# Kernel tuning notes

Hardware: AMD Instinct MI355X
Metric: run time of the kernel (lower is better)

## Reference

```python
import jax, jax.numpy as jnp
import numpy as np

N, F_IN, H = 8192, 128, 256
AVG_DEG_P = 16.0 / N  # ~16 neighbors per node, BA-graph-like sparsity


def setup_inputs() -> dict:
    key = jax.random.key(0)
    ks = jax.random.split(key, 16)
    # symmetric 0/1 adjacency, no self-loops
    B = jax.random.bernoulli(ks[0], AVG_DEG_P, (N, N)).astype(jnp.float32)
    A = jnp.maximum(B, B.T)
    A = A * (1.0 - jnp.eye(N, dtype=jnp.float32))
    features = jax.random.normal(ks[1], (N, F_IN), dtype=jnp.float32)
    treatments = jax.random.bernoulli(ks[2], 0.1, (N, 1)).astype(jnp.float32)
    def glorot(k, shape):
        lim = float(np.sqrt(6.0 / (shape[0] + shape[1])))
        return jax.random.uniform(k, shape, jnp.float32, -lim, lim)
    return {
        "A": A,
        "features": features,
        "treatments": treatments,
        "W1": glorot(ks[3], (F_IN, H)),   # GCNConv layer 1 weight
        "b1": jnp.zeros((H,), jnp.float32),
        "W2": glorot(ks[4], (H, H)),      # GCNConv layer 2 weight
        "b2": jnp.zeros((H,), jnp.float32),
        "W_emb": glorot(ks[5], (H + 1, H)),
        "b_emb": jnp.zeros((H,), jnp.float32),
        "W_t0": glorot(ks[6], (H, 1)),
        "b_t0": jnp.zeros((1,), jnp.float32),
        "W_t1": glorot(ks[7], (H, 1)),
        "b_t1": jnp.zeros((1,), jnp.float32),
    }


def _gcn_norm(A):
    # PyG GCNConv default: D^-1/2 (A + I) D^-1/2
    A_hat = A + jnp.eye(A.shape[0], dtype=A.dtype)
    d = jnp.sum(A_hat, axis=1)
    dinv = jnp.where(d > 0, 1.0 / jnp.sqrt(d), 0.0)
    return A_hat * dinv[:, None] * dinv[None, :]


def reference(A, features, treatments, W1, b1, W2, b2, W_emb, b_emb, W_t0, b_t0, W_t1, b_t1):
    nA = _gcn_norm(A)                                  # [N, N]
    h = jax.nn.relu(nA @ (features @ W1) + b1)         # GCNConv 1, [N, H]
    h = jax.nn.relu(nA @ (h @ W2) + b2)                # GCNConv 2, [N, H]
    deg = jnp.sum(A, axis=1) + 1e-8                    # [N]
    # faithful to torch: (A * treatments).sum(dim=1) broadcasts treatments[N,1] over columns
    exposure = (jnp.sum(A * treatments, axis=1) / deg)[:, None]  # [N, 1]
    rep = jnp.concatenate([h, exposure], axis=1)       # [N, H+1]
    emb = jax.nn.relu(rep @ W_emb + b_emb)             # [N, H]
    y0_pred = (emb @ W_t0 + b_t0).reshape(-1)          # [N]
    y1_pred = (emb @ W_t1 + b_t1).reshape(-1)          # [N]
    return (y0_pred, y1_pred, emb)
```

## Files before the change

kernel.cpp:

```cpp
#include <hip/hip_runtime.h>

#define NN   8192
#define FIN  128
#define HH   256
#define CAP  128

typedef float f32x4 __attribute__((ext_vector_type(4)));

__device__ __forceinline__ const f32x4* c4(const float* p) { return (const f32x4*)p; }
__device__ __forceinline__       f32x4* p4(float* p)       { return (f32x4*)p; }

__device__ __forceinline__ void build_body(
    int row, const float* __restrict__ A, const float* __restrict__ treat,
    int* __restrict__ cols, int* __restrict__ cnt,
    float* __restrict__ dinv, float* __restrict__ expo,
    int* s_cnt, float* s_rs)
{
  const f32x4* Ar = c4(A + (size_t)row * NN);
  if (threadIdx.x == 0) *s_cnt = 0;
  __syncthreads();

  float rs = 0.f;
  int* myCols = cols + (size_t)row * CAP;
  #pragma unroll
  for (int it = 0; it < NN / 4 / 256; ++it) {
    const int idx = it * 256 + threadIdx.x;
    const f32x4 a = __builtin_nontemporal_load(Ar + idx);
    const int base = idx * 4;
    #pragma unroll
    for (int u = 0; u < 4; ++u) {
      if (a[u] != 0.0f) {
        rs += a[u];
        int p = atomicAdd(s_cnt, 1);
        if (p < CAP) myCols[p] = base + u;
      }
    }
  }
  #pragma unroll
  for (int off = 32; off > 0; off >>= 1) rs += __shfl_down(rs, off);
  const int wid = threadIdx.x >> 6;
  if ((threadIdx.x & 63) == 0) s_rs[wid] = rs;
  __syncthreads();
  if (threadIdx.x == 0) {
    const float R = s_rs[0] + s_rs[1] + s_rs[2] + s_rs[3];
    int n = *s_cnt; if (n > CAP) n = CAP;
    cnt[row]  = n;
    dinv[row] = rsqrtf(R + 1.0f);
    expo[row] = treat[row] * R / (R + 1e-8f);
  }
}

template<int K, bool EXPO, bool HEADS>
__device__ __forceinline__ void gemm_body(
    int bidx,
    const float* __restrict__ M, const float* __restrict__ W,
    const float* __restrict__ bias, const float* __restrict__ expo,
    const float* __restrict__ Wt0, const float* __restrict__ Wt1,
    float* __restrict__ out, float* __restrict__ y0, float* __restrict__ y1,
    float (*As)[64], float (*Bs)[64])
{
  const int tid = threadIdx.x;
  const int tx = tid & 15, ty = tid >> 4;
  const int bx = bidx & 127, by = bidx >> 7;
  const int r0 = bx * 64, c0 = by * 64;
  const int la_r = tid & 63;
  const int la_k = (tid >> 6) << 2;
  const int lb_k = tid >> 4;
  const int lb_c = (tid & 15) << 2;

  const float* Abase = M + (size_t)(r0 + la_r) * K + la_k;
  const float* Bbase = W + (size_t)lb_k * HH + c0 + lb_c;

  f32x4 aR = *c4(Abase);
  f32x4 bR = *c4(Bbase);
  float acc[4][4] = {};

  #pragma unroll 1
  for (int k0 = 0; k0 < K; k0 += 16) {
    As[la_k + 0][la_r] = aR[0];
    As[la_k + 1][la_r] = aR[1];
    As[la_k + 2][la_r] = aR[2];
    As[la_k + 3][la_r] = aR[3];
    *p4(&Bs[lb_k][lb_c]) = bR;
    __syncthreads();
    if (k0 + 16 < K) {
      aR = *c4(Abase + k0 + 16);
      bR = *c4(Bbase + (size_t)(k0 + 16) * HH);
    }
    #pragma unroll
    for (int kk = 0; kk < 16; ++kk) {
      const f32x4 av = *c4(&As[kk][ty * 4]);
      const f32x4 bv = *c4(&Bs[kk][tx * 4]);
      #pragma unroll
      for (int i = 0; i < 4; ++i)
        #pragma unroll
        for (int j = 0; j < 4; ++j)
          acc[i][j] += av[i] * bv[j];
    }
    __syncthreads();
  }

  f32x4 eb = {0.f, 0.f, 0.f, 0.f}, bs = {0.f, 0.f, 0.f, 0.f};
  if constexpr (EXPO) {
    eb = *c4(&W[(size_t)K * HH + c0 + tx * 4]);
    bs = *c4(&bias[c0 + tx * 4]);
  }
  f32x4 wt0 = {0.f, 0.f, 0.f, 0.f}, wt1 = {0.f, 0.f, 0.f, 0.f};
  if constexpr (HEADS) {
    wt0 = *c4(&Wt0[c0 + tx * 4]);
    wt1 = *c4(&Wt1[c0 + tx * 4]);
  }
  #pragma unroll
  for (int i = 0; i < 4; ++i) {
    const int r = r0 + ty * 4 + i;
    f32x4 o;
    if constexpr (EXPO) {
      const float e = expo[r];
      #pragma unroll
      for (int j = 0; j < 4; ++j) o[j] = fmaxf(acc[i][j] + e * eb[j] + bs[j], 0.f);
    } else {
      #pragma unroll
      for (int j = 0; j < 4; ++j) o[j] = acc[i][j];
    }
    *p4(&out[(size_t)r * HH + c0 + tx * 4]) = o;
    if constexpr (HEADS) {
      float s0 = o[0] * wt0[0] + o[1] * wt0[1] + o[2] * wt0[2] + o[3] * wt0[3];
      float s1 = o[0] * wt1[0] + o[1] * wt1[1] + o[2] * wt1[2] + o[3] * wt1[3];
      #pragma unroll
      for (int off = 8; off > 0; off >>= 1) {
        s0 += __shfl_down(s0, off);
        s1 += __shfl_down(s1, off);
      }
      if ((tid & 15) == 0) {
        atomicAdd(&y0[r], s0);
        atomicAdd(&y1[r], s1);
      }
    }
  }
}

__global__ __launch_bounds__(256) void k_build_gemm1(
    const float* __restrict__ A, const float* __restrict__ treat,
    const float* __restrict__ feats, const float* __restrict__ W1,
    int* __restrict__ cols, int* __restrict__ cnt,
    float* __restrict__ dinv, float* __restrict__ expo,
    float* __restrict__ bufA)
{
  __shared__ float As[16][64];
  __shared__ float Bs[16][64];
  __shared__ int   s_cnt;
  __shared__ float s_rs[4];
  const int b = blockIdx.x;
  if (b < 512) {
    gemm_body<FIN, false, false>(b, feats, W1, nullptr, nullptr, nullptr, nullptr,
                                 bufA, nullptr, nullptr, As, Bs);
  } else {
    build_body(b - 512, A, treat, cols, cnt, dinv, expo, &s_cnt, s_rs);
  }
}

template<int K, bool EXPO, bool HEADS>
__global__ __launch_bounds__(256) void k_gemm(
    const float* __restrict__ M, const float* __restrict__ W,
    const float* __restrict__ bias, const float* __restrict__ expo,
    const float* __restrict__ Wt0, const float* __restrict__ Wt1,
    float* __restrict__ out, float* __restrict__ y0, float* __restrict__ y1)
{
  __shared__ float As[16][64];
  __shared__ float Bs[16][64];
  gemm_body<K, EXPO, HEADS>(blockIdx.x, M, W, bias, expo, Wt0, Wt1, out, y0, y1, As, Bs);
}

template<bool INIT>
__global__ __launch_bounds__(256) void k_agg(
    const float* __restrict__ M,
    const int* __restrict__ cols, const int* __restrict__ cnt,
    const float* __restrict__ dinv, const float* __restrict__ bias,
    float* __restrict__ out,
    float* __restrict__ dout, const float* __restrict__ bt0, const float* __restrict__ bt1)
{
  const int wid  = threadIdx.x >> 6;
  const int lane = threadIdx.x & 63;
  const int i    = blockIdx.x * 4 + wid;
  __shared__ int   s_cols[4][CAP];
  __shared__ float s_w[4][CAP];

  if constexpr (INIT) {
    if (blockIdx.x < 64) {
      const int idx = blockIdx.x * 256 + threadIdx.x;
      dout[idx] = (idx < NN) ? bt0[0] : bt1[0];
    }
  }

  const int n = cnt[i];
  if (lane < n) {
    const int j = cols[(size_t)i * CAP + lane];
    s_cols[wid][lane] = j;  s_w[wid][lane] = dinv[j];
  }
  if (lane + 64 < n) {
    const int j = cols[(size_t)i * CAP + lane + 64];
    s_cols[wid][lane + 64] = j;  s_w[wid][lane + 64] = dinv[j];
  }
  __syncthreads();

  const float di = dinv[i];
  const f32x4 bias4 = *c4(&bias[lane * 4]);
  f32x4 acc = *c4(&M[(size_t)i * HH + lane * 4]);
  acc *= di;
  #pragma unroll 4
  for (int t = 0; t < n; ++t) {
    const int   j = s_cols[wid][t];
    const float w = s_w[wid][t];
    const f32x4 v = *c4(&M[(size_t)j * HH + lane * 4]);
    acc += w * v;
  }
  f32x4 o = di * acc + bias4;
  #pragma unroll
  for (int q = 0; q < 4; ++q) o[q] = fmaxf(o[q], 0.f);
  *p4(&out[(size_t)i * HH + lane * 4]) = o;
}

extern "C" void kernel_launch(void* const* d_in, const int* in_sizes, int n_in,
                              void* d_out, int out_size, void* d_ws, size_t ws_size,
                              hipStream_t stream)
{
  const float* A      = (const float*)d_in[0];
  const float* feats  = (const float*)d_in[1];
  const float* treat  = (const float*)d_in[2];
  const float* W1     = (const float*)d_in[3];
  const float* b1     = (const float*)d_in[4];
  const float* W2     = (const float*)d_in[5];
  const float* b2     = (const float*)d_in[6];
  const float* W_emb  = (const float*)d_in[7];
  const float* b_emb  = (const float*)d_in[8];
  const float* W_t0   = (const float*)d_in[9];
  const float* b_t0   = (const float*)d_in[10];
  const float* W_t1   = (const float*)d_in[11];
  const float* b_t1   = (const float*)d_in[12];
  float* dout = (float*)d_out;

  int*   cols = (int*)d_ws;
  int*   cnt  = cols + (size_t)NN * CAP;
  float* dinv = (float*)(cnt + NN);
  float* expo = dinv + NN;
  float* bufA = expo + NN;
  float* bufB = bufA + (size_t)NN * HH;

  float* y0  = dout;
  float* y1  = dout + NN;
  float* emb = dout + 2 * NN;

  k_build_gemm1<<<8704, 256, 0, stream>>>(A, treat, feats, W1, cols, cnt, dinv, expo, bufA);
  k_agg<false><<<NN / 4, 256, 0, stream>>>(bufA, cols, cnt, dinv, b1, bufB,
                                           nullptr, nullptr, nullptr);
  k_gemm<HH, false, false><<<512, 256, 0, stream>>>(bufB, W2, nullptr, nullptr,
                                                    nullptr, nullptr, bufA, nullptr, nullptr);
  k_agg<true><<<NN / 4, 256, 0, stream>>>(bufA, cols, cnt, dinv, b2, bufB,
                                          dout, b_t0, b_t1);
  k_gemm<HH, true, true><<<512, 256, 0, stream>>>(bufB, W_emb, b_emb, expo,
                                                  W_t0, W_t1, emb, y0, y1);
}
```

Before: 458.4 us.

## Reorder GCN layer 1 to aggregate 128-wide features before the W1 GEMM

Result: faster. 441.0 us (-3.8%).

```diff
diff --git a/kernel.cpp b/kernel.cpp
--- a/kernel.cpp
+++ b/kernel.cpp
@@ -6,18 +6,23 @@
 #define CAP  128
 
 typedef float f32x4 __attribute__((ext_vector_type(4)));
+typedef float f32x2 __attribute__((ext_vector_type(2)));
 
 __device__ __forceinline__ const f32x4* c4(const float* p) { return (const f32x4*)p; }
 __device__ __forceinline__       f32x4* p4(float* p)       { return (f32x4*)p; }
-
-__device__ __forceinline__ void build_body(
-    int row, const float* __restrict__ A, const float* __restrict__ treat,
+__device__ __forceinline__ const f32x2* c2(const float* p) { return (const f32x2*)p; }
+__device__ __forceinline__       f32x2* p2(float* p)       { return (f32x2*)p; }
+
+__global__ __launch_bounds__(256) void k_build(
+    const float* __restrict__ A, const float* __restrict__ treat,
     int* __restrict__ cols, int* __restrict__ cnt,
-    float* __restrict__ dinv, float* __restrict__ expo,
-    int* s_cnt, float* s_rs)
-{
+    float* __restrict__ dinv, float* __restrict__ expo)
+{
+  const int row = blockIdx.x;
   const f32x4* Ar = c4(A + (size_t)row * NN);
-  if (threadIdx.x == 0) *s_cnt = 0;
+  __shared__ int   s_cnt;
+  __shared__ float s_rs[4];
+  if (threadIdx.x == 0) s_cnt = 0;
   __syncthreads();
 
   float rs = 0.f;
@@ -31,7 +36,7 @@
     for (int u = 0; u < 4; ++u) {
       if (a[u] != 0.0f) {
         rs += a[u];
-        int p = atomicAdd(s_cnt, 1);
+        int p = atomicAdd(&s_cnt, 1);
         if (p < CAP) myCols[p] = base + u;
       }
     }
@@ -43,14 +48,48 @@
   __syncthreads();
   if (threadIdx.x == 0) {
     const float R = s_rs[0] + s_rs[1] + s_rs[2] + s_rs[3];
-    int n = *s_cnt; if (n > CAP) n = CAP;
+    int n = s_cnt; if (n > CAP) n = CAP;
     cnt[row]  = n;
     dinv[row] = rsqrtf(R + 1.0f);
     expo[row] = treat[row] * R / (R + 1e-8f);
   }
 }
 
-template<int K, bool EXPO, bool HEADS>
+__global__ __launch_bounds__(256) void k_agg0(
+    const float* __restrict__ X,
+    const int* __restrict__ cols, const int* __restrict__ cnt,
+    const float* __restrict__ dinv, float* __restrict__ out)
+{
+  const int wid  = threadIdx.x >> 6;
+  const int lane = threadIdx.x & 63;
+  const int i    = blockIdx.x * 4 + wid;
+  __shared__ int   s_cols[4][CAP];
+  __shared__ float s_w[4][CAP];
+
+  const int n = cnt[i];
+  if (lane < n) {
+    const int j = cols[(size_t)i * CAP + lane];
+    s_cols[wid][lane] = j;  s_w[wid][lane] = dinv[j];
+  }
+  if (lane + 64 < n) {
+    const int j = cols[(size_t)i * CAP + lane + 64];
+    s_cols[wid][lane + 64] = j;  s_w[wid][lane + 64] = dinv[j];
+  }
+  __syncthreads();
+
+  const float di = dinv[i];
+  f32x2 acc = *c2(&X[(size_t)i * FIN + lane * 2]);
+  acc *= di;
+  #pragma unroll 4
+  for (int t = 0; t < n; ++t) {
+    const int   j = s_cols[wid][t];
+    const float w = s_w[wid][t];
+    acc += w * (*c2(&X[(size_t)j * FIN + lane * 2]));
+  }
+  *p2(&out[(size_t)i * FIN + lane * 2]) = di * acc;
+}
+
+template<int K, bool RELU, bool EXPO, bool HEADS>
 __device__ __forceinline__ void gemm_body(
     int bidx,
     const float* __restrict__ M, const float* __restrict__ W,
@@ -101,10 +140,8 @@
   }
 
   f32x4 eb = {0.f, 0.f, 0.f, 0.f}, bs = {0.f, 0.f, 0.f, 0.f};
-  if constexpr (EXPO) {
-    eb = *c4(&W[(size_t)K * HH + c0 + tx * 4]);
-    bs = *c4(&bias[c0 + tx * 4]);
-  }
+  if constexpr (RELU) bs = *c4(&bias[c0 + tx * 4]);
+  if constexpr (EXPO) eb = *c4(&W[(size_t)K * HH + c0 + tx * 4]);
   f32x4 wt0 = {0.f, 0.f, 0.f, 0.f}, wt1 = {0.f, 0.f, 0.f, 0.f};
   if constexpr (HEADS) {
     wt0 = *c4(&Wt0[c0 + tx * 4]);
@@ -114,10 +151,15 @@
   for (int i = 0; i < 4; ++i) {
     const int r = r0 + ty * 4 + i;
     f32x4 o;
-    if constexpr (EXPO) {
-      const float e = expo[r];
-      #pragma unroll
-      for (int j = 0; j < 4; ++j) o[j] = fmaxf(acc[i][j] + e * eb[j] + bs[j], 0.f);
+    if constexpr (RELU) {
+      float e = 0.f;
+      if constexpr (EXPO) e = expo[r];
+      #pragma unroll
+      for (int j = 0; j < 4; ++j) {
+        float v = acc[i][j] + bs[j];
+        if constexpr (EXPO) v += e * eb[j];
+        o[j] = fmaxf(v, 0.f);
+      }
     } else {
       #pragma unroll
       for (int j = 0; j < 4; ++j) o[j] = acc[i][j];
@@ -139,27 +181,7 @@
   }
 }
 
-__global__ __launch_bounds__(256) void k_build_gemm1(
-    const float* __restrict__ A, const float* __restrict__ treat,
-    const float* __restrict__ feats, const float* __restrict__ W1,
-    int* __restrict__ cols, int* __restrict__ cnt,
-    float* __restrict__ dinv, float* __restrict__ expo,
-    float* __restrict__ bufA)
-{
-  __shared__ float As[16][64];
-  __shared__ float Bs[16][64];
-  __shared__ int   s_cnt;
-  __shared__ float s_rs[4];
-  const int b = blockIdx.x;
-  if (b < 512) {
-    gemm_body<FIN, false, false>(b, feats, W1, nullptr, nullptr, nullptr, nullptr,
-                                 bufA, nullptr, nullptr, As, Bs);
-  } else {
-    build_body(b - 512, A, treat, cols, cnt, dinv, expo, &s_cnt, s_rs);
-  }
-}
-
-template<int K, bool EXPO, bool HEADS>
+template<int K, bool RELU, bool EXPO, bool HEADS>
 __global__ __launch_bounds__(256) void k_gemm(
     const float* __restrict__ M, const float* __restrict__ W,
     const float* __restrict__ bias, const float* __restrict__ expo,
@@ -168,7 +190,8 @@
 {
   __shared__ float As[16][64];
   __shared__ float Bs[16][64];
-  gemm_body<K, EXPO, HEADS>(blockIdx.x, M, W, bias, expo, Wt0, Wt1, out, y0, y1, As, Bs);
+  gemm_body<K, RELU, EXPO, HEADS>(blockIdx.x, M, W, bias, expo, Wt0, Wt1,
+                                  out, y0, y1, As, Bs);
 }
 
 template<bool INIT>
@@ -211,8 +234,7 @@
   for (int t = 0; t < n; ++t) {
     const int   j = s_cols[wid][t];
     const float w = s_w[wid][t];
-    const f32x4 v = *c4(&M[(size_t)j * HH + lane * 4]);
-    acc += w * v;
+    acc += w * (*c4(&M[(size_t)j * HH + lane * 4]));
   }
   f32x4 o = di * acc + bias4;
   #pragma unroll
@@ -243,20 +265,22 @@
   int*   cnt  = cols + (size_t)NN * CAP;
   float* dinv = (float*)(cnt + NN);
   float* expo = dinv + NN;
-  float* bufA = expo + NN;
+  float* bufX = expo + NN;
+  float* bufA = bufX + (size_t)NN * FIN;
   float* bufB = bufA + (size_t)NN * HH;
 
   float* y0  = dout;
   float* y1  = dout + NN;
   float* emb = dout + 2 * NN;
 
-  k_build_gemm1<<<8704, 256, 0, stream>>>(A, treat, feats, W1, cols, cnt, dinv, expo, bufA);
-  k_agg<false><<<NN / 4, 256, 0, stream>>>(bufA, cols, cnt, dinv, b1, bufB,
-                                           nullptr, nullptr, nullptr);
-  k_gemm<HH, false, false><<<512, 256, 0, stream>>>(bufB, W2, nullptr, nullptr,
-                                                    nullptr, nullptr, bufA, nullptr, nullptr);
+  k_build<<<NN, 256, 0, stream>>>(A, treat, cols, cnt, dinv, expo);
+  k_agg0<<<NN / 4, 256, 0, stream>>>(feats, cols, cnt, dinv, bufX);
+  k_gemm<FIN, true, false, false><<<512, 256, 0, stream>>>(
+      bufX, W1, b1, nullptr, nullptr, nullptr, bufB, nullptr, nullptr);
+  k_gemm<HH, false, false, false><<<512, 256, 0, stream>>>(
+      bufB, W2, nullptr, nullptr, nullptr, nullptr, bufA, nullptr, nullptr);
   k_agg<true><<<NN / 4, 256, 0, stream>>>(bufA, cols, cnt, dinv, b2, bufB,
                                           dout, b_t0, b_t1);
-  k_gemm<HH, true, true><<<512, 256, 0, stream>>>(bufB, W_emb, b_emb, expo,
-                                                  W_t0, W_t1, emb, y0, y1);
-}
+  k_gemm<HH, true, true, true><<<512, 256, 0, stream>>>(
+      bufB, W_emb, b_emb, expo, W_t0, W_t1, emb, y0, y1);
+}
```
